# Kernel tuning notes

Measured on AMD Instinct MI355X. Metric: run time of the kernel, lower is better.

Reference implementation:

```python
import jax, jax.numpy as jnp
import numpy as np

B, KB, SEQ, HID = 8, 16, 512, 768  # batch, two_times_batch, max_length, hidden
NEG_INF = float('-inf')


def _l2_normalize(x, eps=1e-12):
    # torch F.normalize: x / max(||x||_2, eps)
    n = jnp.sqrt(jnp.sum(x * x, axis=-1, keepdims=True))
    return x / jnp.maximum(n, eps)


def setup_inputs() -> dict:
    key = jax.random.key(0)
    k1, k2, k3, k4 = jax.random.split(key, 4)
    return {
        'query_embs': jax.random.normal(k1, (B, SEQ, HID), dtype=jnp.float32),
        'key_embs': jax.random.normal(k2, (KB, SEQ, HID), dtype=jnp.float32),
        'alpha_raw': jnp.float32(0.1),  # learnable scalar, cfg.model.alpha init
        'q_mask': jax.random.randint(k3, (B, SEQ), 0, 2, dtype=jnp.int32),
        'k_mask': jax.random.randint(k4, (KB, SEQ), 0, 2, dtype=jnp.int32),
    }


def reference(query_embs, key_embs, alpha_raw, q_mask, k_mask):
    # cfg: distance_weightning='exp', use_softmax=True, gumbel_temp=None
    qn = _l2_normalize(query_embs)          # [B, S, H]
    kn = _l2_normalize(key_embs)            # [KB, T, H]

    # cosine similarity: [B, KB, S, T]
    sim = jnp.einsum('ish,jth->ijst', qn, kn)

    # exp distance weighting, alpha = leaky_relu(alpha_raw)
    alpha = jax.nn.leaky_relu(alpha_raw)
    pos = jnp.arange(SEQ, dtype=jnp.float32)
    distance = jnp.abs(pos[:, None] - pos[None, :])        # [S, T]
    sim = sim * jnp.exp(-alpha * distance)

    valid = (q_mask[:, None, :, None] != 0) & (k_mask[None, :, None, :] != 0)
    logits = jnp.where(valid, sim, NEG_INF)

    p = jax.nn.softmax(logits, axis=-1)                    # [B, KB, S, T]
    p = jnp.nan_to_num(p, nan=0.0)

    # aggregate normalized keys under attention, dot with queries
    aggregated = jnp.einsum('ijst,jth->ijsh', p, kn)       # [B, KB, S, H]
    scores = jnp.einsum('ish,ijsh->ijs', qn, aggregated)   # [B, KB, S]
    scores = scores * q_mask[:, None, :].astype(scores.dtype)
    return scores.sum(axis=-1)                             # [B, KB]
```

## Files before the change

kernel.cpp:

```cpp
#include <hip/hip_runtime.h>
#include <stdint.h>

#define B_   8
#define KB_  16
#define SEQ_ 512
#define HID_ 768

#define NKB  (HID_ / 32)
#define QRB  (B_  * SEQ_ / 16)
#define KRB  (KB_ * SEQ_ / 16)

typedef __attribute__((ext_vector_type(4))) _Float16 half4;
typedef __attribute__((ext_vector_type(8))) _Float16 half8;
typedef __attribute__((ext_vector_type(4))) float    floatx4;

#define GLOBAL_AS __attribute__((address_space(1)))
#define LDS_AS    __attribute__((address_space(3)))

static __device__ __forceinline__ void async_tile16(const _Float16* g, _Float16* l)
{
    __builtin_amdgcn_global_load_lds((const GLOBAL_AS uint32_t*)g,
                                     (LDS_AS uint32_t*)l, 16, 0, 0);
}

#define LP 776

__global__ __launch_bounds__(256)
void prep_tile(const float* __restrict__ Q, const float* __restrict__ K,
               _Float16* __restrict__ Qt, _Float16* __restrict__ Kt)
{
    const int rb = blockIdx.x;
    const float* src;
    _Float16*    dst;
    if (rb < QRB) { src = Q + (size_t)rb * 16 * HID_;          dst = Qt + (size_t)rb * NKB * 512; }
    else          { src = K + (size_t)(rb - QRB) * 16 * HID_;  dst = Kt + (size_t)(rb - QRB) * NKB * 512; }

    __shared__ _Float16 Ls[16 * LP];
    const int wave = threadIdx.x >> 6;
    const int lane = threadIdx.x & 63;

#pragma unroll
    for (int rr = 0; rr < 4; ++rr) {
        int row = wave * 4 + rr;
        const float* s = src + (size_t)row * HID_;
        float4 v[3];
        float ss = 0.f;
#pragma unroll
        for (int it = 0; it < 3; ++it) {
            v[it] = *(const float4*)(s + lane * 4 + it * 256);
            ss += v[it].x * v[it].x + v[it].y * v[it].y + v[it].z * v[it].z + v[it].w * v[it].w;
        }
#pragma unroll
        for (int m = 1; m < 64; m <<= 1) ss += __shfl_xor(ss, m, 64);
        float sc = 1.0f / fmaxf(sqrtf(ss), 1e-12f);
#pragma unroll
        for (int it = 0; it < 3; ++it) {
            half4 h = { (_Float16)(v[it].x * sc), (_Float16)(v[it].y * sc),
                        (_Float16)(v[it].z * sc), (_Float16)(v[it].w * sc) };
            *(half4*)(Ls + row * LP + lane * 4 + it * 256) = h;
        }
    }
    __syncthreads();

#pragma unroll
    for (int rep = 0; rep < 6; ++rep) {
        int slot = rep * 256 + threadIdx.x;
        int kb   = slot >> 6;
        int ln   = slot & 63;
        int row  = ln & 15;
        int ko   = kb * 32 + (ln >> 4) * 8;
        half8 h = *(const half8*)(Ls + row * LP + ko);
        *(half8*)(dst + (size_t)kb * 512 + (size_t)ln * 8) = h;
    }
}

__global__ __launch_bounds__(512, 4)
void li_part(const _Float16* __restrict__ Qt, const _Float16* __restrict__ Kt,
             const float* __restrict__ alpha_p, const int* __restrict__ kmask,
             float* __restrict__ Pbuf)
{
    const int st = blockIdx.x >> 1;
    const int tb = blockIdx.x & 1;
    const int j  = blockIdx.y;
    const int i  = blockIdx.z;

    const int tid  = threadIdx.x;
    const int lane = tid & 63;
    const int wave = tid >> 6;
    const int quad = lane >> 4;
    const int l16  = lane & 15;
    const int wr   = wave >> 2;
    const int wc   = wave & 3;

    __shared__ _Float16 Sbuf[2][24 * 512];
    __shared__ float lred[4][128], nred[4][128];

    const float araw  = *alpha_p;
    const float alpha = araw >= 0.f ? araw : 0.01f * araw;

    const int qbase = i * 32 + st * 8;
    const int kbase = j * 32 + tb * 16;

    const _Float16* gsrc[3];
    _Float16*       ldst0[3];
#pragma unroll
    for (int q = 0; q < 3; ++q) {
        int t   = wave * 3 + q;
        int rbg = (t < 8) ? (qbase + t) : (kbase + (t - 8));
        const _Float16* base = (t < 8) ? Qt : Kt;
        gsrc[q]  = base + (size_t)rbg * NKB * 512 + (size_t)lane * 8;
        ldst0[q] = &Sbuf[0][t * 512];
    }

    floatx4 acc[4][4];
#pragma unroll
    for (int rt = 0; rt < 4; ++rt)
#pragma unroll
        for (int ct = 0; ct < 4; ++ct)
            acc[rt][ct] = (floatx4){0.f, 0.f, 0.f, 0.f};

#pragma unroll
    for (int q = 0; q < 3; ++q)
        async_tile16(gsrc[q], ldst0[q]);

    for (int kb = 0; kb < NKB; ++kb) {
        const int b = kb & 1;
        __syncthreads();
        if (kb + 1 < NKB) {
#pragma unroll
            for (int q = 0; q < 3; ++q)
                async_tile16(gsrc[q] + (size_t)(kb + 1) * 512, ldst0[q] + (b ^ 1) * 24 * 512);
        }
        const _Float16* Qs = &Sbuf[b][0];
        const _Float16* Ks = &Sbuf[b][8 * 512];
        half8 af[4], bf[4];
#pragma unroll
        for (int rt = 0; rt < 4; ++rt)
            af[rt] = *(const half8*)(Qs + (wr * 4 + rt) * 512 + lane * 8);
#pragma unroll
        for (int ct = 0; ct < 4; ++ct)
            bf[ct] = *(const half8*)(Ks + (wc * 4 + ct) * 512 + lane * 8);
#pragma unroll
        for (int rt = 0; rt < 4; ++rt)
#pragma unroll
            for (int ct = 0; ct < 4; ++ct)
                acc[rt][ct] = __builtin_amdgcn_mfma_f32_16x16x32_f16(af[rt], bf[ct], acc[rt][ct], 0, 0, 0);
    }

    const int* km = kmask + j * SEQ_ + tb * 256;
    int kmv[4]; float tgf[4];
#pragma unroll
    for (int ct = 0; ct < 4; ++ct) {
        int t_loc = wc * 64 + ct * 16 + l16;
        kmv[ct] = km[t_loc];
        tgf[ct] = (float)(tb * 256 + t_loc);
    }
#pragma unroll
    for (int rt = 0; rt < 4; ++rt) {
#pragma unroll
        for (int r = 0; r < 4; ++r) {
            float sgf = (float)(st * 128 + wr * 64 + rt * 16 + quad * 4 + r);
            float ps = 0.f, ns = 0.f;
#pragma unroll
            for (int ct = 0; ct < 4; ++ct) {
                float cv = acc[rt][ct][r];
                float e  = kmv[ct] ? __expf(cv * __expf(-alpha * fabsf(sgf - tgf[ct]))) : 0.f;
                ps += e;
                ns += e * cv;
            }
#pragma unroll
            for (int msk = 1; msk < 16; msk <<= 1) {
                ps += __shfl_xor(ps, msk, 64);
                ns += __shfl_xor(ns, msk, 64);
            }
            if (l16 == 0) {
                int rloc = wr * 64 + rt * 16 + quad * 4 + r;
                lred[wc][rloc] = ps;
                nred[wc][rloc] = ns;
            }
        }
    }
    __syncthreads();

    if (tid < 128) {
        float l = lred[0][tid] + lred[1][tid] + lred[2][tid] + lred[3][tid];
        float n = nred[0][tid] + nred[1][tid] + nred[2][tid] + nred[3][tid];
        size_t base = (((size_t)(i * KB_ + j) * SEQ_) + st * 128 + tid) * 4 + tb * 2;
        Pbuf[base]     = l;
        Pbuf[base + 1] = n;
    }
}

__global__ __launch_bounds__(256)
void li_reduce(const float* __restrict__ Pbuf, const int* __restrict__ qmask,
               float* __restrict__ out)
{
    const int ij = blockIdx.x;
    const int i  = ij >> 4;
    const int tid = threadIdx.x;
    __shared__ float red[4];

    float sum = 0.f;
#pragma unroll
    for (int rep = 0; rep < 2; ++rep) {
        int s = tid + rep * 256;
        float4 a = *(const float4*)(Pbuf + ((size_t)ij * SEQ_ + s) * 4);
        float l = a.x + a.z;
        float n = a.y + a.w;
        float sc = (l > 0.f) ? n / l : 0.f;
        if (qmask[i * SEQ_ + s] == 0) sc = 0.f;
        sum += sc;
    }
#pragma unroll
    for (int m = 1; m < 64; m <<= 1) sum += __shfl_xor(sum, m, 64);
    if ((tid & 63) == 0) red[tid >> 6] = sum;
    __syncthreads();
    if (tid == 0) out[ij] = red[0] + red[1] + red[2] + red[3];
}

extern "C" void kernel_launch(void* const* d_in, const int* in_sizes, int n_in,
                              void* d_out, int out_size, void* d_ws, size_t ws_size,
                              hipStream_t stream)
{
    const float* Q       = (const float*)d_in[0];
    const float* K       = (const float*)d_in[1];
    const float* alpha_p = (const float*)d_in[2];
    const int*   qmask   = (const int*)d_in[3];
    const int*   kmask   = (const int*)d_in[4];
    float*       out     = (float*)d_out;

    char* ws = (char*)d_ws;
    _Float16* Qt   = (_Float16*)ws;
    _Float16* Kt   = (_Float16*)(ws + (size_t)B_ * SEQ_ * HID_ * 2);
    float*    Pbuf = (float*)   (ws + (size_t)(B_ + KB_) * SEQ_ * HID_ * 2);

    prep_tile<<<QRB + KRB, 256, 0, stream>>>(Q, K, Qt, Kt);

    dim3 grid(8, KB_, B_);
    li_part<<<grid, 512, 0, stream>>>(Qt, Kt, alpha_p, kmask, Pbuf);

    li_reduce<<<B_ * KB_, 256, 0, stream>>>(Pbuf, qmask, out);
}
```

Before: 141.1 us.

## Widen main tile to full key row and fuse reduction via atomics

Each block now covers all 512 key positions for its 128-query chunk, so the two per-t-half partial sums no longer need merging and the partial buffer goes away. The separate reduce kernel is folded into the main kernel, which adds its masked per-row scores into the output with an atomicAdd after a memset. This removes one launch and the global round trip, and loads each Q tile once instead of twice. In exchange it doubles the accumulator registers and LDS per block (occupancy hint drops from 4 to 2) and halves the grid to 512 blocks.

```diff
diff --git a/kernel.cpp b/kernel.cpp
--- a/kernel.cpp
+++ b/kernel.cpp
@@ -74,13 +74,12 @@
     }
 }
 
-__global__ __launch_bounds__(512, 4)
-void li_part(const _Float16* __restrict__ Qt, const _Float16* __restrict__ Kt,
+__global__ __launch_bounds__(512, 2)
+void li_main(const _Float16* __restrict__ Qt, const _Float16* __restrict__ Kt,
              const float* __restrict__ alpha_p, const int* __restrict__ kmask,
-             float* __restrict__ Pbuf)
-{
-    const int st = blockIdx.x >> 1;
-    const int tb = blockIdx.x & 1;
+             const int* __restrict__ qmask, float* __restrict__ out)
+{
+    const int st = blockIdx.x;
     const int j  = blockIdx.y;
     const int i  = blockIdx.z;
 
@@ -92,35 +91,36 @@
     const int wr   = wave >> 2;
     const int wc   = wave & 3;
 
-    __shared__ _Float16 Sbuf[2][24 * 512];
+    __shared__ _Float16 Sbuf[2][40 * 512];
     __shared__ float lred[4][128], nred[4][128];
+    __shared__ float sred[2];
 
     const float araw  = *alpha_p;
     const float alpha = araw >= 0.f ? araw : 0.01f * araw;
 
     const int qbase = i * 32 + st * 8;
-    const int kbase = j * 32 + tb * 16;
-
-    const _Float16* gsrc[3];
-    _Float16*       ldst0[3];
-#pragma unroll
-    for (int q = 0; q < 3; ++q) {
-        int t   = wave * 3 + q;
+    const int kbase = j * 32;
+
+    const _Float16* gsrc[5];
+    _Float16*       ldst0[5];
+#pragma unroll
+    for (int q = 0; q < 5; ++q) {
+        int t   = wave * 5 + q;
         int rbg = (t < 8) ? (qbase + t) : (kbase + (t - 8));
         const _Float16* base = (t < 8) ? Qt : Kt;
         gsrc[q]  = base + (size_t)rbg * NKB * 512 + (size_t)lane * 8;
         ldst0[q] = &Sbuf[0][t * 512];
     }
 
-    floatx4 acc[4][4];
+    floatx4 acc[4][8];
 #pragma unroll
     for (int rt = 0; rt < 4; ++rt)
 #pragma unroll
-        for (int ct = 0; ct < 4; ++ct)
+        for (int ct = 0; ct < 8; ++ct)
             acc[rt][ct] = (floatx4){0.f, 0.f, 0.f, 0.f};
 
 #pragma unroll
-    for (int q = 0; q < 3; ++q)
+    for (int q = 0; q < 5; ++q)
         async_tile16(gsrc[q], ldst0[q]);
 
     for (int kb = 0; kb < NKB; ++kb) {
@@ -128,32 +128,32 @@
         __syncthreads();
         if (kb + 1 < NKB) {
 #pragma unroll
-            for (int q = 0; q < 3; ++q)
-                async_tile16(gsrc[q] + (size_t)(kb + 1) * 512, ldst0[q] + (b ^ 1) * 24 * 512);
+            for (int q = 0; q < 5; ++q)
+                async_tile16(gsrc[q] + (size_t)(kb + 1) * 512, ldst0[q] + (b ^ 1) * 40 * 512);
         }
         const _Float16* Qs = &Sbuf[b][0];
         const _Float16* Ks = &Sbuf[b][8 * 512];
-        half8 af[4], bf[4];
+        half8 af[4], bf[8];
 #pragma unroll
         for (int rt = 0; rt < 4; ++rt)
             af[rt] = *(const half8*)(Qs + (wr * 4 + rt) * 512 + lane * 8);
 #pragma unroll
-        for (int ct = 0; ct < 4; ++ct)
-            bf[ct] = *(const half8*)(Ks + (wc * 4 + ct) * 512 + lane * 8);
+        for (int ct = 0; ct < 8; ++ct)
+            bf[ct] = *(const half8*)(Ks + (wc * 8 + ct) * 512 + lane * 8);
 #pragma unroll
         for (int rt = 0; rt < 4; ++rt)
 #pragma unroll
-            for (int ct = 0; ct < 4; ++ct)
+            for (int ct = 0; ct < 8; ++ct)
                 acc[rt][ct] = __builtin_amdgcn_mfma_f32_16x16x32_f16(af[rt], bf[ct], acc[rt][ct], 0, 0, 0);
     }
 
-    const int* km = kmask + j * SEQ_ + tb * 256;
-    int kmv[4]; float tgf[4];
-#pragma unroll
-    for (int ct = 0; ct < 4; ++ct) {
-        int t_loc = wc * 64 + ct * 16 + l16;
+    const int* km = kmask + j * SEQ_;
+    int kmv[8]; float tgf[8];
+#pragma unroll
+    for (int ct = 0; ct < 8; ++ct) {
+        int t_loc = wc * 128 + ct * 16 + l16;
         kmv[ct] = km[t_loc];
-        tgf[ct] = (float)(tb * 256 + t_loc);
+        tgf[ct] = (float)t_loc;
     }
 #pragma unroll
     for (int rt = 0; rt < 4; ++rt) {
@@ -162,7 +162,7 @@
             float sgf = (float)(st * 128 + wr * 64 + rt * 16 + quad * 4 + r);
             float ps = 0.f, ns = 0.f;
 #pragma unroll
-            for (int ct = 0; ct < 4; ++ct) {
+            for (int ct = 0; ct < 8; ++ct) {
                 float cv = acc[rt][ct][r];
                 float e  = kmv[ct] ? __expf(cv * __expf(-alpha * fabsf(sgf - tgf[ct]))) : 0.f;
                 ps += e;
@@ -182,40 +182,21 @@
     }
     __syncthreads();
 
+    float sum = 0.f;
     if (tid < 128) {
         float l = lred[0][tid] + lred[1][tid] + lred[2][tid] + lred[3][tid];
         float n = nred[0][tid] + nred[1][tid] + nred[2][tid] + nred[3][tid];
-        size_t base = (((size_t)(i * KB_ + j) * SEQ_) + st * 128 + tid) * 4 + tb * 2;
-        Pbuf[base]     = l;
-        Pbuf[base + 1] = n;
-    }
-}
-
-__global__ __launch_bounds__(256)
-void li_reduce(const float* __restrict__ Pbuf, const int* __restrict__ qmask,
-               float* __restrict__ out)
-{
-    const int ij = blockIdx.x;
-    const int i  = ij >> 4;
-    const int tid = threadIdx.x;
-    __shared__ float red[4];
-
-    float sum = 0.f;
-#pragma unroll
-    for (int rep = 0; rep < 2; ++rep) {
-        int s = tid + rep * 256;
-        float4 a = *(const float4*)(Pbuf + ((size_t)ij * SEQ_ + s) * 4);
-        float l = a.x + a.z;
-        float n = a.y + a.w;
         float sc = (l > 0.f) ? n / l : 0.f;
-        if (qmask[i * SEQ_ + s] == 0) sc = 0.f;
-        sum += sc;
-    }
-#pragma unroll
-    for (int m = 1; m < 64; m <<= 1) sum += __shfl_xor(sum, m, 64);
-    if ((tid & 63) == 0) red[tid >> 6] = sum;
+        if (qmask[i * SEQ_ + st * 128 + tid] == 0) sc = 0.f;
+        sum = sc;
+    }
+    if (tid < 128) {
+#pragma unroll
+        for (int m = 1; m < 64; m <<= 1) sum += __shfl_xor(sum, m, 64);
+        if (lane == 0) sred[wave] = sum;
+    }
     __syncthreads();
-    if (tid == 0) out[ij] = red[0] + red[1] + red[2] + red[3];
+    if (tid == 0) atomicAdd(out + i * KB_ + j, sred[0] + sred[1]);
 }
 
 extern "C" void kernel_launch(void* const* d_in, const int* in_sizes, int n_in,
@@ -230,14 +211,13 @@
     float*       out     = (float*)d_out;
 
     char* ws = (char*)d_ws;
-    _Float16* Qt   = (_Float16*)ws;
-    _Float16* Kt   = (_Float16*)(ws + (size_t)B_ * SEQ_ * HID_ * 2);
-    float*    Pbuf = (float*)   (ws + (size_t)(B_ + KB_) * SEQ_ * HID_ * 2);
+    _Float16* Qt = (_Float16*)ws;
+    _Float16* Kt = (_Float16*)(ws + (size_t)B_ * SEQ_ * HID_ * 2);
+
+    hipMemsetAsync(d_out, 0, (size_t)out_size * sizeof(float), stream);
 
     prep_tile<<<QRB + KRB, 256, 0, stream>>>(Q, K, Qt, Kt);
 
-    dim3 grid(8, KB_, B_);
-    li_part<<<grid, 512, 0, stream>>>(Qt, Kt, alpha_p, kmask, Pbuf);
-
-    li_reduce<<<B_ * KB_, 256, 0, stream>>>(Pbuf, qmask, out);
-}
+    dim3 grid(SEQ_ / 128, KB_, B_);
+    li_main<<<grid, 512, 0, stream>>>(Qt, Kt, alpha_p, kmask, qmask, out);
+}
```

New measurement: 163.1 us. 1.16x slower.
